# Kernel optimization log

Measured on AMD Instinct MI355X. Metric: run time of the kernel, lower is better.

The kernel has to match this reference:

```python
import jax, jax.numpy as jnp
import numpy as np

D = 128      # dim_hidden
L = 8        # topological levels (level 0 = primary inputs)
M = 32768    # nodes per level
N = L * M
G = 5        # gate types: maj/not/and/or/xor -> 5 param sets
F = 2        # fan-in per gate node


def setup_inputs() -> dict:
    key = jax.random.key(0)
    ks = jax.random.split(key, 18)
    p = lambda k, sh: jax.random.normal(k, sh, jnp.float32) * 0.05
    return {
        's': jax.random.normal(ks[0], (N, D), jnp.float32),
        't': jax.random.normal(ks[1], (N, D), jnp.float32),
        'gate': jax.random.randint(ks[2], (N,), 0, G, jnp.int32),
        'fanin': jax.random.randint(ks[3], (L - 1, M, F), 0, M, jnp.int32),
        'hs_W': p(ks[4], (2 * D, D)), 'hs_b': p(ks[5], (D,)),
        'aggr_W1': p(ks[6], (G, 2 * D, D)), 'aggr_b1': p(ks[7], (G, D)),
        'aggr_W2': p(ks[8], (G, D, D)), 'aggr_b2': p(ks[9], (G, D)),
        'aggr_W3': p(ks[10], (G, D, D)), 'aggr_b3': p(ks[11], (G, D)),
        'gru_Wi': p(ks[12], (G, D, 3 * D)), 'gru_Wh': p(ks[13], (G, D, 3 * D)),
        'gru_bi': p(ks[14], (G, 3 * D)), 'gru_bh': p(ks[15], (G, 3 * D)),
    }


def _forward(s, t, gate, fanin, hs_W, hs_b, aggr_W1, aggr_b1, aggr_W2, aggr_b2,
             aggr_W3, aggr_b3, gru_Wi, gru_Wh, gru_bi, gru_bh):
    hs = jnp.concatenate([s, t], -1) @ hs_W + hs_b          # [N,D]
    hf = jnp.zeros((N, D), hs.dtype)                        # functional state, zero-init
    for lvl in range(1, L):                                 # level-synchronous sweep
        lo = lvl * M
        g_l = gate[lo:lo + M]                               # [M] gate type of dst nodes
        oh = jax.nn.one_hot(g_l, G, dtype=hs.dtype)         # [M,G] gate selector
        src = (lvl - 1) * M + fanin[lvl - 1]                # [M,F] global fan-in indices
        src_state = jnp.concatenate([hs[src], hf[src]], -1)  # [M,F,2D] node_state gather
        # per-gate-type edge MLP (TFMlpAggr): 3-layer MLP on source states, sum over fan-in
        h1 = jax.nn.relu(jnp.einsum('mfc,gcd->gmfd', src_state, aggr_W1) + aggr_b1[:, None, None, :])
        h2 = jax.nn.relu(jnp.einsum('gmfd,gde->gmfe', h1, aggr_W2) + aggr_b2[:, None, None, :])
        m = jnp.einsum('gmfe,gek->gmfk', h2, aggr_W3) + aggr_b3[:, None, None, :]
        msg = jnp.einsum('gmd,mg->md', m.sum(axis=2), oh)   # [M,D] select own gate's aggr
        # per-gate-type GRU update of hf (torch GRU math, seq_len=1)
        h = hf[lo:lo + M]                                   # [M,D]
        gi = jnp.einsum('md,gdk->gmk', msg, gru_Wi) + gru_bi[:, None, :]  # [G,M,3D]
        gh = jnp.einsum('md,gdk->gmk', h, gru_Wh) + gru_bh[:, None, :]
        r = jax.nn.sigmoid(gi[..., :D] + gh[..., :D])
        z = jax.nn.sigmoid(gi[..., D:2 * D] + gh[..., D:2 * D])
        n = jnp.tanh(gi[..., 2 * D:] + r * gh[..., 2 * D:])
        h_new = jnp.einsum('gmd,mg->md', (1.0 - z) * n + z * h[None], oh)
        hf = hf.at[lo:lo + M].set(h_new)                    # scatter-write back
    return hs, hf


def reference(s, t, gate, fanin, hs_W, hs_b, aggr_W1, aggr_b1, aggr_W2, aggr_b2,
              aggr_W3, aggr_b3, gru_Wi, gru_Wh, gru_bi, gru_bh):
    return _forward(s, t, gate, fanin, hs_W, hs_b, aggr_W1, aggr_b1, aggr_W2,
                    aggr_b2, aggr_W3, aggr_b3, gru_Wi, gru_Wh, gru_bi, gru_bh)
```

## Files before the change

### kernel.cpp

```cpp
#include <hip/hip_runtime.h>
#include <hip/hip_bf16.h>

#define DD 128
#define LL 8
#define MM 32768
#define NN (LL*MM)
#define GG 5
#define FF 2
#define SORT_STRIDE 33408

typedef __attribute__((ext_vector_type(8))) short short8;
typedef __attribute__((ext_vector_type(4))) short short4v;
typedef __attribute__((ext_vector_type(4))) float f32x4;

#define MFMA16(a,b,c) __builtin_amdgcn_mfma_f32_16x16x32_bf16((a),(b),(c),0,0,0)
#define VMEM_FENCE() asm volatile("s_waitcnt vmcnt(0)" ::: "memory")

__device__ __forceinline__ short f2bf(float x){
  __hip_bfloat16 h = __float2bfloat16(x);
  return *reinterpret_cast<short*>(&h);
}

__device__ __forceinline__ short8 pack8(f32x4 a, f32x4 b){
  short8 r;
  r[0]=f2bf(a[0]); r[1]=f2bf(a[1]); r[2]=f2bf(a[2]); r[3]=f2bf(a[3]);
  r[4]=f2bf(b[0]); r[5]=f2bf(b[1]); r[6]=f2bf(b[2]); r[7]=f2bf(b[3]);
  return r;
}

__global__ void prep_kernel(const float* __restrict__ hs_W, const float* __restrict__ W1,
                            const float* __restrict__ W2, const float* __restrict__ W3,
                            const float* __restrict__ Wi,
                            short* __restrict__ hsWt, short* __restrict__ W1t,
                            short* __restrict__ W2t, short* __restrict__ W3t,
                            short* __restrict__ Wit, int* __restrict__ cntcur)
{
  if (blockIdx.x == 0 && threadIdx.x < 70) cntcur[threadIdx.x] = 0;
  int u = blockIdx.x*256 + threadIdx.x;
  const float* src; short* dst; int ldw;
  if (u < 4096){
    int i=u, ct=i>>9, kc=(i>>6)&7, ln=i&63;
    src = hs_W + (size_t)(kc*32 + 8*(ln>>4))*128 + ct*16 + (ln&15);
    dst = hsWt + (size_t)i*8; ldw=128;
  } else if (u < 24576){
    int v=u-4096, g=v>>12, i=v&4095, ct=i>>9, kc=(i>>6)&7, ln=i&63;
    src = W1 + (size_t)g*32768 + (size_t)(kc*32 + 8*(ln>>4))*128 + ct*16 + (ln&15);
    dst = W1t + (size_t)g*32768 + i*8; ldw=128;
  } else if (u < 34816){
    int v=u-24576, g=v>>11, i=v&2047, ct=i>>8, kc=(i>>6)&3, ln=i&63;
    src = W2 + (size_t)g*16384 + (size_t)(kc*32 + 8*(ln>>4))*128 + ct*16 + (ln&15);
    dst = W2t + (size_t)g*16384 + i*8; ldw=128;
  } else if (u < 45056){
    int v=u-34816, g=v>>11, i=v&2047, ct=i>>8, kc=(i>>6)&3, ln=i&63;
    src = W3 + (size_t)g*16384 + (size_t)(kc*32 + 8*(ln>>4))*128 + ct*16 + (ln&15);
    dst = W3t + (size_t)g*16384 + i*8; ldw=128;
  } else {
    int v=u-45056, g=v/6144, i=v%6144, ct=i>>8, kc=(i>>6)&3, ln=i&63;
    src = Wi + (size_t)g*49152 + (size_t)(kc*32 + 8*(ln>>4))*384 + ct*16 + (ln&15);
    dst = Wit + (size_t)g*49152 + i*8; ldw=384;
  }
  short8 o;
#pragma unroll
  for (int j=0;j<8;++j) o[j] = f2bf(src[(size_t)j*ldw]);
  *(short8*)dst = o;
}

__global__ void count_kernel(const int* __restrict__ gate, int* __restrict__ cnt){
  __shared__ int lc[GG];
  const int li = blockIdx.x >> 7;
  const int m  = ((blockIdx.x & 127) << 8) + threadIdx.x;
  if (threadIdx.x < GG) lc[threadIdx.x] = 0;
  __syncthreads();
  int g = gate[(li+1)*MM + m];
  atomicAdd(&lc[g], 1);
  __syncthreads();
  if (threadIdx.x < GG && lc[threadIdx.x] > 0)
    atomicAdd(&cnt[li*GG + threadIdx.x], lc[threadIdx.x]);
}

__global__ void offs_kernel(const int* __restrict__ cnt, int* __restrict__ off,
                            int* __restrict__ pend, int* __restrict__ sorted){
  __shared__ int se[35], sp[35];
  const int tid = threadIdx.x;
  if (tid < LL-1){
    int l = tid, o = 0;
    for (int g = 0; g < GG; ++g){
      off[l*GG+g] = o;
      int c = cnt[l*GG+g];
      pend[l*GG+g] = o + c;
      se[l*GG+g] = o + c;
      o += ((c + 31) >> 5) << 5;
      sp[l*GG+g] = o;
    }
  }
  __syncthreads();
  for (int b = 0; b < 35; ++b){
    int l = b / GG;
    for (int i = se[b] + tid; i < sp[b]; i += 256)
      sorted[l*SORT_STRIDE + i] = -1;
  }
}

__global__ void scatter_kernel(const int* __restrict__ gate, const int* __restrict__ off,
                               int* __restrict__ cur, int* __restrict__ sorted){
  __shared__ int lc[GG];
  __shared__ int base[GG];
  const int li = blockIdx.x >> 7;
  const int m  = ((blockIdx.x & 127) << 8) + threadIdx.x;
  if (threadIdx.x < GG) lc[threadIdx.x] = 0;
  __syncthreads();
  int g = gate[(li+1)*MM + m];
  int p = atomicAdd(&lc[g], 1);
  __syncthreads();
  if (threadIdx.x < GG)
    base[threadIdx.x] = atomicAdd(&cur[li*GG + threadIdx.x], lc[threadIdx.x]);
  __syncthreads();
  sorted[li*SORT_STRIDE + off[li*GG+g] + base[g] + p] = m;
}

__global__ __launch_bounds__(256,5) void hs_kernel(
    const float* __restrict__ s, const float* __restrict__ t,
    const short* __restrict__ Wt, const float* __restrict__ b,
    float* __restrict__ hs, short* __restrict__ xsh,
    float* __restrict__ hf)
{
  __shared__ __align__(16) short Xs[16384];
  const int tid=threadIdx.x, lane=tid&63, w=tid>>6;
  const int l15=lane&15, lq=lane>>4;
  const int row0 = blockIdx.x*64;

  {
    const int r = tid>>2, p = tid&3;
    const float* srow = s + (size_t)(row0+r)*DD;
    const float* trow = t + (size_t)(row0+r)*DD;
    const int rf = r>>4, rl = r&15;
#pragma unroll
    for (int h=0; h<2; ++h){
      f32x4 va[8];
#pragma unroll
      for (int i=0;i<4;++i){
        int u = p + 4*(4*h + i);
        const float* pp = (u<16) ? (srow + 8*u) : (trow + 8*(u-16));
        va[2*i]   = __builtin_nontemporal_load((const f32x4*)pp);
        va[2*i+1] = __builtin_nontemporal_load((const f32x4*)(pp+4));
      }
      VMEM_FENCE();
#pragma unroll
      for (int i=0;i<4;++i){
        int u = p + 4*(4*h + i);
        short8 v = pack8(va[2*i], va[2*i+1]);
        *(short8*)(Xs + ((rf*8+(u>>2))*64 + (u&3)*16 + rl)*8) = v;
      }
    }
  }

  if (row0 < MM){
    f32x4 zf4 = {0.f,0.f,0.f,0.f};
    short8 zs8 = {0,0,0,0,0,0,0,0};
    const size_t basei = (size_t)row0*DD;
    for (int i=tid; i<2048; i+=256)
      __builtin_nontemporal_store(zf4, (f32x4*)(hf + basei + i*4));
    for (int i=tid; i<1024; i+=256)
      *(short8*)(xsh + ((size_t)row0 + (i>>4))*256 + 128 + (i&15)*8) = zs8;
  }
  __syncthreads();

  f32x4 zf = {0.f,0.f,0.f,0.f};
  f32x4 acc[4][2];
#pragma unroll
  for (int rr=0;rr<4;++rr){ acc[rr][0]=zf; acc[rr][1]=zf; }
  const short* Aw = Wt + (16*w)*512 + lane*8;
#pragma unroll
  for (int h=0; h<2; ++h){
    short8 af[8];
#pragma unroll
    for (int i=0;i<8;++i) af[i] = *(const short8*)(Aw + (8*h + i)*512);
    VMEM_FENCE();
#pragma unroll
    for (int kc=0;kc<8;++kc){
      short8 bx[4];
#pragma unroll
      for (int rr=0;rr<4;++rr)
        bx[rr] = *(const short8*)(Xs + ((rr*8 + kc)*64 + lane)*8);
#pragma unroll
      for (int rr=0;rr<4;++rr)
        acc[rr][h] = MFMA16(af[kc], bx[rr], acc[rr][h]);
    }
  }

  f32x4 bv0 = *(const f32x4*)(b + 32*w + 4*lq);
  f32x4 bv1 = *(const f32x4*)(b + 32*w + 16 + 4*lq);
#pragma unroll
  for (int rr=0;rr<4;++rr){
    int row = row0 + rr*16 + l15;
#pragma unroll
    for (int q=0;q<2;++q){
      f32x4 bv = q ? bv1 : bv0;
      int col = 32*w + 16*q + 4*lq;
      f32x4 o; short4v pk;
#pragma unroll
      for (int j=0;j<4;++j){ o[j] = acc[rr][q][j] + bv[j]; pk[j] = f2bf(o[j]); }
      __builtin_nontemporal_store(o, (f32x4*)(hs + (size_t)row*DD + col));
      *(short4v*)(xsh + (size_t)row*256 + col) = pk;
    }
  }
}

__global__ __launch_bounds__(256,5) void level_kernel(
    int lvl, float* __restrict__ hfg, short* __restrict__ xsh,
    const int* __restrict__ fanin,
    const short* __restrict__ W1t, const short* __restrict__ W2t,
    const short* __restrict__ W3t, const short* __restrict__ Wit,
    const float* __restrict__ b1, const float* __restrict__ b2,
    const float* __restrict__ b3, const float* __restrict__ bi,
    const float* __restrict__ bh,
    const int* __restrict__ off, const int* __restrict__ pend,
    const int* __restrict__ sorted)
{
  __shared__ __align__(16) short Xs[16384];
  const int tid=threadIdx.x, lane=tid&63, w=tid>>6;
  const int l15=lane&15, lq=lane>>4;
  const int li = lvl-1;

  const int bid = blockIdx.x;
  const int xcd = bid & 7, idx = bid >> 3;
  const int nbid = ((xcd < 4) ? xcd*131 : 524 + (xcd-4)*130) + idx;
  const int pos0 = nbid*32;

  int g = -1;
#pragma unroll
  for (int q=0;q<GG;++q)
    if (pos0 >= off[li*GG+q] && pos0 < pend[li*GG+q]) g = q;
  if (g < 0) return;

  const int m0 = sorted[li*SORT_STRIDE + pos0 + l15];
  const int m1 = sorted[li*SORT_STRIDE + pos0 + 16 + l15];
  f32x4 zf = {0.f,0.f,0.f,0.f};

  {
    const int r = tid>>2, p = tid&3;
    const int mg = sorted[li*SORT_STRIDE + pos0 + (r>>1)];
    const int src = (mg>=0) ? li*MM + fanin[((size_t)li*MM+mg)*FF + (r&1)] : 0;
    const short* xrow = xsh + (size_t)src*256;
    const int rf = r>>4, rl = r&15;
    const bool lvl1 = (lvl == 1);
    short8 va[8];
    short8 zs8 = {0,0,0,0,0,0,0,0};
#pragma unroll
    for (int i=0;i<8;++i){
      int u = p + 4*i;
      va[i] = (lvl1 && u >= 16) ? zs8 : *(const short8*)(xrow + 8*u);
    }
    VMEM_FENCE();
#pragma unroll
    for (int i=0;i<8;++i){
      int u = p + 4*i;
      *(short8*)(Xs + ((rf*8+(u>>2))*64 + (u&3)*16 + rl)*8) = va[i];
    }
  }
  __syncthreads();

  f32x4 acc[4][2];
#pragma unroll
  for (int rr=0;rr<4;++rr){ acc[rr][0]=zf; acc[rr][1]=zf; }
  {
    const short* A1w = W1t + (size_t)g*32768 + (16*w)*512 + lane*8;
#pragma unroll
    for (int h=0; h<2; ++h){
      short8 af[8];
#pragma unroll
      for (int i=0;i<8;++i) af[i] = *(const short8*)(A1w + (8*h + i)*512);
      VMEM_FENCE();
#pragma unroll
      for (int kc=0;kc<8;++kc){
        short8 bx[4];
#pragma unroll
        for (int rr=0;rr<4;++rr)
          bx[rr] = *(const short8*)(Xs + ((rr*8 + kc)*64 + lane)*8);
#pragma unroll
        for (int rr=0;rr<4;++rr)
          acc[rr][h] = MFMA16(af[kc], bx[rr], acc[rr][h]);
      }
    }
  }
  __syncthreads();
  {
    f32x4 bv0 = *(const f32x4*)(b1 + g*DD + 32*w + 4*lq);
    f32x4 bv1 = *(const f32x4*)(b1 + g*DD + 32*w + 16 + 4*lq);
#pragma unroll
    for (int rr=0;rr<4;++rr){
#pragma unroll
      for (int q=0;q<2;++q){
        f32x4 bv = q ? bv1 : bv0;
        short4v pk;
#pragma unroll
        for (int j=0;j<4;++j) pk[j] = f2bf(fmaxf(acc[rr][q][j] + bv[j], 0.f));
        *(short4v*)(Xs + ((rr*4 + w)*64 + (2*q + (lq>>1))*16 + l15)*8 + 4*(lq&1)) = pk;
      }
    }
  }
  __syncthreads();

  f32x4 acc2[4][2];
#pragma unroll
  for (int rr=0;rr<4;++rr){ acc2[rr][0]=zf; acc2[rr][1]=zf; }
  {
    const short* A2w = W2t + (size_t)g*16384 + (8*w)*512 + lane*8;
    short8 af[8];
#pragma unroll
    for (int i=0;i<8;++i) af[i] = *(const short8*)(A2w + i*512);
    VMEM_FENCE();
#pragma unroll
    for (int kc=0;kc<4;++kc){
      short8 bx[4];
#pragma unroll
      for (int rr=0;rr<4;++rr)
        bx[rr] = *(const short8*)(Xs + ((rr*4 + kc)*64 + lane)*8);
#pragma unroll
      for (int rr=0;rr<4;++rr){
        acc2[rr][0] = MFMA16(af[kc],   bx[rr], acc2[rr][0]);
        acc2[rr][1] = MFMA16(af[4+kc], bx[rr], acc2[rr][1]);
      }
    }
  }
  {
    f32x4 bv0 = *(const f32x4*)(b2 + g*DD + 32*w + 4*lq);
    f32x4 bv1 = *(const f32x4*)(b2 + g*DD + 32*w + 16 + 4*lq);
#pragma unroll
    for (int rr=0;rr<4;++rr){
#pragma unroll
      for (int q=0;q<2;++q){
        f32x4 bv = q ? bv1 : bv0;
        short4v pk;
#pragma unroll
        for (int j=0;j<4;++j) pk[j] = f2bf(fmaxf(acc2[rr][q][j] + bv[j], 0.f));
        *(short4v*)(Xs + 8192 + ((rr*4 + w)*64 + (2*q + (lq>>1))*16 + l15)*8 + 4*(lq&1)) = pk;
      }
    }
  }
  __syncthreads();

  f32x4 acc3[4][2];
#pragma unroll
  for (int rr=0;rr<4;++rr){ acc3[rr][0]=zf; acc3[rr][1]=zf; }
  {
    const short* A3w = W3t + (size_t)g*16384 + (8*w)*512 + lane*8;
    short8 af[8];
#pragma unroll
    for (int i=0;i<8;++i) af[i] = *(const short8*)(A3w + i*512);
    VMEM_FENCE();
#pragma unroll
    for (int kc=0;kc<4;++kc){
      short8 bx[4];
#pragma unroll
      for (int rr=0;rr<4;++rr)
        bx[rr] = *(const short8*)(Xs + 8192 + ((rr*4 + kc)*64 + lane)*8);
#pragma unroll
      for (int rr=0;rr<4;++rr){
        acc3[rr][0] = MFMA16(af[kc],   bx[rr], acc3[rr][0]);
        acc3[rr][1] = MFMA16(af[4+kc], bx[rr], acc3[rr][1]);
      }
    }
  }
  {
    f32x4 bv0 = *(const f32x4*)(b3 + g*DD + 32*w + 4*lq);
    f32x4 bv1 = *(const f32x4*)(b3 + g*DD + 32*w + 16 + 4*lq);
#pragma unroll
    for (int rr=0;rr<4;++rr){
#pragma unroll
      for (int q=0;q<2;++q){
        f32x4 bv = q ? bv1 : bv0;
        f32x4 mv;
#pragma unroll
        for (int j=0;j<4;++j){
          float v = acc3[rr][q][j];
          mv[j] = v + __shfl_xor(v, 1) + 2.f*bv[j];
        }
        if ((l15 & 1) == 0){
          int n = rr*8 + (l15>>1);
          short4v pk;
#pragma unroll
          for (int j=0;j<4;++j) pk[j] = f2bf(mv[j]);
          *(short4v*)(Xs + (((n>>4)*4 + w)*64 + (2*q + (lq>>1))*16 + (n&15))*8 + 4*(lq&1)) = pk;
        }
      }
    }
  }
  __syncthreads();

  const short* AW = Wit + (size_t)g*49152 + lane*8;
  const int lo = lvl*MM;
#pragma unroll
  for (int q=0;q<2;++q){
    short8 af[12];
#pragma unroll
    for (int kc=0;kc<4;++kc){
      int cti = ((2*w + q)*4 + kc)*512;
      af[kc]   = *(const short8*)(AW + cti);
      af[4+kc] = *(const short8*)(AW + 16384 + cti);
      af[8+kc] = *(const short8*)(AW + 32768 + cti);
    }
    VMEM_FENCE();
    f32x4 gr[2], gz[2], gn[2];
    gr[0]=zf; gr[1]=zf; gz[0]=zf; gz[1]=zf; gn[0]=zf; gn[1]=zf;
#pragma unroll
    for (int kc=0;kc<4;++kc){
#pragma unroll
      for (int rfm=0;rfm<2;++rfm){
        short8 bm = *(const short8*)(Xs + ((rfm*4 + kc)*64 + lane)*8);
        gr[rfm] = MFMA16(af[kc],   bm, gr[rfm]);
        gz[rfm] = MFMA16(af[4+kc], bm, gz[rfm]);
        gn[rfm] = MFMA16(af[8+kc], bm, gn[rfm]);
      }
    }
    int col = 32*w + 16*q + 4*lq;
    f32x4 biR = *(const f32x4*)(bi + g*384 + col);
    f32x4 biZ = *(const f32x4*)(bi + g*384 + 128 + col);
    f32x4 biN = *(const f32x4*)(bi + g*384 + 256 + col);
    f32x4 bhR = *(const f32x4*)(bh + g*384 + col);
    f32x4 bhZ = *(const f32x4*)(bh + g*384 + 128 + col);
    f32x4 bhN = *(const f32x4*)(bh + g*384 + 256 + col);
#pragma unroll
    for (int rfm=0;rfm<2;++rfm){
      int m = rfm ? m1 : m0;
      if (m < 0) continue;
      f32x4 o; short4v pk;
#pragma unroll
      for (int j=0;j<4;++j){
        float xr = gr[rfm][j] + biR[j] + bhR[j];
        float xz = gz[rfm][j] + biZ[j] + bhZ[j];
        float r_ = 1.f/(1.f + __expf(-xr));
        float z_ = 1.f/(1.f + __expf(-xz));
        float xn = gn[rfm][j] + biN[j] + r_*bhN[j];
        float n_ = 2.f/(1.f + __expf(-2.f*xn)) - 1.f;
        o[j] = (1.f - z_)*n_;
        pk[j] = f2bf(o[j]);
      }
      __builtin_nontemporal_store(o, (f32x4*)(hfg + (size_t)(lo + m)*DD + col));
      *(short4v*)(xsh + (size_t)(lo + m)*256 + 128 + col) = pk;
    }
  }
}

extern "C" void kernel_launch(void* const* d_in, const int* in_sizes, int n_in,
                              void* d_out, int out_size, void* d_ws, size_t ws_size,
                              hipStream_t stream)
{
  const float* s    = (const float*)d_in[0];
  const float* t    = (const float*)d_in[1];
  const int*   gate = (const int*)d_in[2];
  const int*   fanin= (const int*)d_in[3];
  const float* hs_W = (const float*)d_in[4];
  const float* hs_b = (const float*)d_in[5];
  const float* W1   = (const float*)d_in[6];
  const float* b1   = (const float*)d_in[7];
  const float* W2   = (const float*)d_in[8];
  const float* b2   = (const float*)d_in[9];
  const float* W3   = (const float*)d_in[10];
  const float* b3   = (const float*)d_in[11];
  const float* Wi   = (const float*)d_in[12];
  const float* bi   = (const float*)d_in[14];
  const float* bh   = (const float*)d_in[15];

  float* hs = (float*)d_out;
  float* hf = hs + (size_t)NN*DD;

  int* cnt    = (int*)d_ws;
  int* cur    = cnt + 35;
  int* off    = cnt + 70;
  int* pendv  = cnt + 105;
  int* sorted = cnt + 256;

  short* wbase = (short*)((char*)d_ws + (1<<20));
  short* hsWt = wbase;
  short* W1t  = wbase + 32768;
  short* W2t  = wbase + 196608;
  short* W3t  = wbase + 278528;
  short* Wit  = wbase + 360448;

  short* xsh = (short*)((char*)d_ws + (size_t)(8<<20));

  prep_kernel<<<296, 256, 0, stream>>>(hs_W, W1, W2, W3, Wi,
                                       hsWt, W1t, W2t, W3t, Wit, cnt);
  count_kernel<<<896, 256, 0, stream>>>(gate, cnt);
  offs_kernel<<<1, 256, 0, stream>>>(cnt, off, pendv, sorted);
  scatter_kernel<<<896, 256, 0, stream>>>(gate, off, cur, sorted);
  hs_kernel<<<NN/64, 256, 0, stream>>>(s, t, hsWt, hs_b, hs, xsh, hf);
  for (int lvl = 1; lvl < LL; ++lvl){
    level_kernel<<<SORT_STRIDE/32, 256, 0, stream>>>(lvl, hf, xsh,
        fanin, W1t, W2t, W3t, Wit,
        b1, b2, b3, bi, bh, off, pendv, sorted);
  }
}
```

Baseline: 378.8 us.

## Process two row tiles per block, prefetching second gather during first compute

Each level-kernel block now handles two consecutive 32-node tiles instead of one, with a halved grid and an adjusted XCD-aware block remapping. The fan-in gather for the second tile is issued into registers before the first tile's MLP+GRU chain runs, so its memory latency overlaps with the first tile's compute. Launch bounds drop from 5 to 4 blocks per CU to make room for the extra prefetch registers, which lowers occupancy and leaves fewer blocks to hide latency.

```diff
diff --git a/kernel.cpp b/kernel.cpp
--- a/kernel.cpp
+++ b/kernel.cpp
@@ -206,7 +206,7 @@
   }
 }
 
-__global__ __launch_bounds__(256,5) void level_kernel(
+__global__ __launch_bounds__(256,4) void level_kernel(
     int lvl, float* __restrict__ hfg, short* __restrict__ xsh,
     const int* __restrict__ fanin,
     const short* __restrict__ W1t, const short* __restrict__ W2t,
@@ -224,221 +224,247 @@
 
   const int bid = blockIdx.x;
   const int xcd = bid & 7, idx = bid >> 3;
-  const int nbid = ((xcd < 4) ? xcd*131 : 524 + (xcd-4)*130) + idx;
-  const int pos0 = nbid*32;
-
-  int g = -1;
-#pragma unroll
-  for (int q=0;q<GG;++q)
-    if (pos0 >= off[li*GG+q] && pos0 < pend[li*GG+q]) g = q;
-  if (g < 0) return;
-
-  const int m0 = sorted[li*SORT_STRIDE + pos0 + l15];
-  const int m1 = sorted[li*SORT_STRIDE + pos0 + 16 + l15];
+  const int nbid = ((xcd < 2) ? xcd*66 : 132 + (xcd-2)*65) + idx;
+  const int pos0 = nbid*64;
+
+  auto lookup_g = [&](int pos) -> int {
+    int g = -1;
+#pragma unroll
+    for (int q=0;q<GG;++q)
+      if (pos >= off[li*GG+q] && pos < pend[li*GG+q]) g = q;
+    return g;
+  };
+  const int g0 = lookup_g(pos0);
+  const int g1 = lookup_g(pos0 + 32);
+
+  const int r = tid>>2, p = tid&3;
+  const int rf = r>>4, rl = r&15;
+  const bool lvl1 = (lvl == 1);
   f32x4 zf = {0.f,0.f,0.f,0.f};
-
-  {
-    const int r = tid>>2, p = tid&3;
-    const int mg = sorted[li*SORT_STRIDE + pos0 + (r>>1)];
+  short8 zs8 = {0,0,0,0,0,0,0,0};
+
+  auto gather_issue = [&](int pos, short8* va){
+    const int mg = sorted[li*SORT_STRIDE + pos + (r>>1)];
     const int src = (mg>=0) ? li*MM + fanin[((size_t)li*MM+mg)*FF + (r&1)] : 0;
     const short* xrow = xsh + (size_t)src*256;
-    const int rf = r>>4, rl = r&15;
-    const bool lvl1 = (lvl == 1);
-    short8 va[8];
-    short8 zs8 = {0,0,0,0,0,0,0,0};
 #pragma unroll
     for (int i=0;i<8;++i){
       int u = p + 4*i;
       va[i] = (lvl1 && u >= 16) ? zs8 : *(const short8*)(xrow + 8*u);
     }
-    VMEM_FENCE();
+  };
+  auto write_xs = [&](const short8* va){
 #pragma unroll
     for (int i=0;i<8;++i){
       int u = p + 4*i;
       *(short8*)(Xs + ((rf*8+(u>>2))*64 + (u&3)*16 + rl)*8) = va[i];
     }
-  }
-  __syncthreads();
-
-  f32x4 acc[4][2];
-#pragma unroll
-  for (int rr=0;rr<4;++rr){ acc[rr][0]=zf; acc[rr][1]=zf; }
-  {
-    const short* A1w = W1t + (size_t)g*32768 + (16*w)*512 + lane*8;
-#pragma unroll
-    for (int h=0; h<2; ++h){
+  };
+
+  auto compute_item = [&](int g, int pos){
+    const int m0 = sorted[li*SORT_STRIDE + pos + l15];
+    const int m1 = sorted[li*SORT_STRIDE + pos + 16 + l15];
+
+    f32x4 acc[4][2];
+#pragma unroll
+    for (int rr=0;rr<4;++rr){ acc[rr][0]=zf; acc[rr][1]=zf; }
+    {
+      const short* A1w = W1t + (size_t)g*32768 + (16*w)*512 + lane*8;
+#pragma unroll
+      for (int h=0; h<2; ++h){
+        short8 af[8];
+#pragma unroll
+        for (int i=0;i<8;++i) af[i] = *(const short8*)(A1w + (8*h + i)*512);
+        VMEM_FENCE();
+#pragma unroll
+        for (int kc=0;kc<8;++kc){
+          short8 bx[4];
+#pragma unroll
+          for (int rr=0;rr<4;++rr)
+            bx[rr] = *(const short8*)(Xs + ((rr*8 + kc)*64 + lane)*8);
+#pragma unroll
+          for (int rr=0;rr<4;++rr)
+            acc[rr][h] = MFMA16(af[kc], bx[rr], acc[rr][h]);
+        }
+      }
+    }
+    __syncthreads();
+    {
+      f32x4 bv0 = *(const f32x4*)(b1 + g*DD + 32*w + 4*lq);
+      f32x4 bv1 = *(const f32x4*)(b1 + g*DD + 32*w + 16 + 4*lq);
+#pragma unroll
+      for (int rr=0;rr<4;++rr){
+#pragma unroll
+        for (int q=0;q<2;++q){
+          f32x4 bv = q ? bv1 : bv0;
+          short4v pk;
+#pragma unroll
+          for (int j=0;j<4;++j) pk[j] = f2bf(fmaxf(acc[rr][q][j] + bv[j], 0.f));
+          *(short4v*)(Xs + ((rr*4 + w)*64 + (2*q + (lq>>1))*16 + l15)*8 + 4*(lq&1)) = pk;
+        }
+      }
+    }
+    __syncthreads();
+
+    f32x4 acc2[4][2];
+#pragma unroll
+    for (int rr=0;rr<4;++rr){ acc2[rr][0]=zf; acc2[rr][1]=zf; }
+    {
+      const short* A2w = W2t + (size_t)g*16384 + (8*w)*512 + lane*8;
       short8 af[8];
 #pragma unroll
-      for (int i=0;i<8;++i) af[i] = *(const short8*)(A1w + (8*h + i)*512);
+      for (int i=0;i<8;++i) af[i] = *(const short8*)(A2w + i*512);
       VMEM_FENCE();
 #pragma unroll
-      for (int kc=0;kc<8;++kc){
+      for (int kc=0;kc<4;++kc){
         short8 bx[4];
 #pragma unroll
         for (int rr=0;rr<4;++rr)
-          bx[rr] = *(const short8*)(Xs + ((rr*8 + kc)*64 + lane)*8);
+          bx[rr] = *(const short8*)(Xs + ((rr*4 + kc)*64 + lane)*8);
+#pragma unroll
+        for (int rr=0;rr<4;++rr){
+          acc2[rr][0] = MFMA16(af[kc],   bx[rr], acc2[rr][0]);
+          acc2[rr][1] = MFMA16(af[4+kc], bx[rr], acc2[rr][1]);
+        }
+      }
+    }
+    {
+      f32x4 bv0 = *(const f32x4*)(b2 + g*DD + 32*w + 4*lq);
+      f32x4 bv1 = *(const f32x4*)(b2 + g*DD + 32*w + 16 + 4*lq);
+#pragma unroll
+      for (int rr=0;rr<4;++rr){
+#pragma unroll
+        for (int q=0;q<2;++q){
+          f32x4 bv = q ? bv1 : bv0;
+          short4v pk;
+#pragma unroll
+          for (int j=0;j<4;++j) pk[j] = f2bf(fmaxf(acc2[rr][q][j] + bv[j], 0.f));
+          *(short4v*)(Xs + 8192 + ((rr*4 + w)*64 + (2*q + (lq>>1))*16 + l15)*8 + 4*(lq&1)) = pk;
+        }
+      }
+    }
+    __syncthreads();
+
+    f32x4 acc3[4][2];
+#pragma unroll
+    for (int rr=0;rr<4;++rr){ acc3[rr][0]=zf; acc3[rr][1]=zf; }
+    {
+      const short* A3w = W3t + (size_t)g*16384 + (8*w)*512 + lane*8;
+      short8 af[8];
+#pragma unroll
+      for (int i=0;i<8;++i) af[i] = *(const short8*)(A3w + i*512);
+      VMEM_FENCE();
+#pragma unroll
+      for (int kc=0;kc<4;++kc){
+        short8 bx[4];
 #pragma unroll
         for (int rr=0;rr<4;++rr)
-          acc[rr][h] = MFMA16(af[kc], bx[rr], acc[rr][h]);
-      }
-    }
-  }
-  __syncthreads();
-  {
-    f32x4 bv0 = *(const f32x4*)(b1 + g*DD + 32*w + 4*lq);
-    f32x4 bv1 = *(const f32x4*)(b1 + g*DD + 32*w + 16 + 4*lq);
-#pragma unroll
-    for (int rr=0;rr<4;++rr){
-#pragma unroll
-      for (int q=0;q<2;++q){
-        f32x4 bv = q ? bv1 : bv0;
-        short4v pk;
-#pragma unroll
-        for (int j=0;j<4;++j) pk[j] = f2bf(fmaxf(acc[rr][q][j] + bv[j], 0.f));
-        *(short4v*)(Xs + ((rr*4 + w)*64 + (2*q + (lq>>1))*16 + l15)*8 + 4*(lq&1)) = pk;
-      }
-    }
-  }
-  __syncthreads();
-
-  f32x4 acc2[4][2];
-#pragma unroll
-  for (int rr=0;rr<4;++rr){ acc2[rr][0]=zf; acc2[rr][1]=zf; }
-  {
-    const short* A2w = W2t + (size_t)g*16384 + (8*w)*512 + lane*8;
-    short8 af[8];
-#pragma unroll
-    for (int i=0;i<8;++i) af[i] = *(const short8*)(A2w + i*512);
+          bx[rr] = *(const short8*)(Xs + 8192 + ((rr*4 + kc)*64 + lane)*8);
+#pragma unroll
+        for (int rr=0;rr<4;++rr){
+          acc3[rr][0] = MFMA16(af[kc],   bx[rr], acc3[rr][0]);
+          acc3[rr][1] = MFMA16(af[4+kc], bx[rr], acc3[rr][1]);
+        }
+      }
+    }
+    {
+      f32x4 bv0 = *(const f32x4*)(b3 + g*DD + 32*w + 4*lq);
+      f32x4 bv1 = *(const f32x4*)(b3 + g*DD + 32*w + 16 + 4*lq);
+#pragma unroll
+      for (int rr=0;rr<4;++rr){
+#pragma unroll
+        for (int q=0;q<2;++q){
+          f32x4 bv = q ? bv1 : bv0;
+          f32x4 mv;
+#pragma unroll
+          for (int j=0;j<4;++j){
+            float v = acc3[rr][q][j];
+            mv[j] = v + __shfl_xor(v, 1) + 2.f*bv[j];
+          }
+          if ((l15 & 1) == 0){
+            int n = rr*8 + (l15>>1);
+            short4v pk;
+#pragma unroll
+            for (int j=0;j<4;++j) pk[j] = f2bf(mv[j]);
+            *(short4v*)(Xs + (((n>>4)*4 + w)*64 + (2*q + (lq>>1))*16 + (n&15))*8 + 4*(lq&1)) = pk;
+          }
+        }
+      }
+    }
+    __syncthreads();
+
+    const short* AW = Wit + (size_t)g*49152 + lane*8;
+    const int lo = lvl*MM;
+#pragma unroll
+    for (int q=0;q<2;++q){
+      short8 af[12];
+#pragma unroll
+      for (int kc=0;kc<4;++kc){
+        int cti = ((2*w + q)*4 + kc)*512;
+        af[kc]   = *(const short8*)(AW + cti);
+        af[4+kc] = *(const short8*)(AW + 16384 + cti);
+        af[8+kc] = *(const short8*)(AW + 32768 + cti);
+      }
+      VMEM_FENCE();
+      f32x4 gr[2], gz[2], gn[2];
+      gr[0]=zf; gr[1]=zf; gz[0]=zf; gz[1]=zf; gn[0]=zf; gn[1]=zf;
+#pragma unroll
+      for (int kc=0;kc<4;++kc){
+#pragma unroll
+        for (int rfm=0;rfm<2;++rfm){
+          short8 bm = *(const short8*)(Xs + ((rfm*4 + kc)*64 + lane)*8);
+          gr[rfm] = MFMA16(af[kc],   bm, gr[rfm]);
+          gz[rfm] = MFMA16(af[4+kc], bm, gz[rfm]);
+          gn[rfm] = MFMA16(af[8+kc], bm, gn[rfm]);
+        }
+      }
+      int col = 32*w + 16*q + 4*lq;
+      f32x4 biR = *(const f32x4*)(bi + g*384 + col);
+      f32x4 biZ = *(const f32x4*)(bi + g*384 + 128 + col);
+      f32x4 biN = *(const f32x4*)(bi + g*384 + 256 + col);
+      f32x4 bhR = *(const f32x4*)(bh + g*384 + col);
+      f32x4 bhZ = *(const f32x4*)(bh + g*384 + 128 + col);
+      f32x4 bhN = *(const f32x4*)(bh + g*384 + 256 + col);
+#pragma unroll
+      for (int rfm=0;rfm<2;++rfm){
+        int m = rfm ? m1 : m0;
+        if (m < 0) continue;
+        f32x4 o; short4v pk;
+#pragma unroll
+        for (int j=0;j<4;++j){
+          float xr = gr[rfm][j] + biR[j] + bhR[j];
+          float xz = gz[rfm][j] + biZ[j] + bhZ[j];
+          float r_ = 1.f/(1.f + __expf(-xr));
+          float z_ = 1.f/(1.f + __expf(-xz));
+          float xn = gn[rfm][j] + biN[j] + r_*bhN[j];
+          float n_ = 2.f/(1.f + __expf(-2.f*xn)) - 1.f;
+          o[j] = (1.f - z_)*n_;
+          pk[j] = f2bf(o[j]);
+        }
+        __builtin_nontemporal_store(o, (f32x4*)(hfg + (size_t)(lo + m)*DD + col));
+        *(short4v*)(xsh + (size_t)(lo + m)*256 + 128 + col) = pk;
+      }
+    }
+  };
+
+  short8 va[8];
+  if (g0 >= 0){
+    gather_issue(pos0, va);
     VMEM_FENCE();
-#pragma unroll
-    for (int kc=0;kc<4;++kc){
-      short8 bx[4];
-#pragma unroll
-      for (int rr=0;rr<4;++rr)
-        bx[rr] = *(const short8*)(Xs + ((rr*4 + kc)*64 + lane)*8);
-#pragma unroll
-      for (int rr=0;rr<4;++rr){
-        acc2[rr][0] = MFMA16(af[kc],   bx[rr], acc2[rr][0]);
-        acc2[rr][1] = MFMA16(af[4+kc], bx[rr], acc2[rr][1]);
-      }
-    }
-  }
-  {
-    f32x4 bv0 = *(const f32x4*)(b2 + g*DD + 32*w + 4*lq);
-    f32x4 bv1 = *(const f32x4*)(b2 + g*DD + 32*w + 16 + 4*lq);
-#pragma unroll
-    for (int rr=0;rr<4;++rr){
-#pragma unroll
-      for (int q=0;q<2;++q){
-        f32x4 bv = q ? bv1 : bv0;
-        short4v pk;
-#pragma unroll
-        for (int j=0;j<4;++j) pk[j] = f2bf(fmaxf(acc2[rr][q][j] + bv[j], 0.f));
-        *(short4v*)(Xs + 8192 + ((rr*4 + w)*64 + (2*q + (lq>>1))*16 + l15)*8 + 4*(lq&1)) = pk;
-      }
-    }
-  }
-  __syncthreads();
-
-  f32x4 acc3[4][2];
-#pragma unroll
-  for (int rr=0;rr<4;++rr){ acc3[rr][0]=zf; acc3[rr][1]=zf; }
-  {
-    const short* A3w = W3t + (size_t)g*16384 + (8*w)*512 + lane*8;
-    short8 af[8];
-#pragma unroll
-    for (int i=0;i<8;++i) af[i] = *(const short8*)(A3w + i*512);
+    write_xs(va);
+  }
+  __syncthreads();
+  if (g1 >= 0){
+    gather_issue(pos0 + 32, va);
+    __builtin_amdgcn_sched_barrier(0);
+  }
+  if (g0 >= 0) compute_item(g0, pos0);
+  __syncthreads();
+  if (g1 >= 0){
     VMEM_FENCE();
-#pragma unroll
-    for (int kc=0;kc<4;++kc){
-      short8 bx[4];
-#pragma unroll
-      for (int rr=0;rr<4;++rr)
-        bx[rr] = *(const short8*)(Xs + 8192 + ((rr*4 + kc)*64 + lane)*8);
-#pragma unroll
-      for (int rr=0;rr<4;++rr){
-        acc3[rr][0] = MFMA16(af[kc],   bx[rr], acc3[rr][0]);
-        acc3[rr][1] = MFMA16(af[4+kc], bx[rr], acc3[rr][1]);
-      }
-    }
-  }
-  {
-    f32x4 bv0 = *(const f32x4*)(b3 + g*DD + 32*w + 4*lq);
-    f32x4 bv1 = *(const f32x4*)(b3 + g*DD + 32*w + 16 + 4*lq);
-#pragma unroll
-    for (int rr=0;rr<4;++rr){
-#pragma unroll
-      for (int q=0;q<2;++q){
-        f32x4 bv = q ? bv1 : bv0;
-        f32x4 mv;
-#pragma unroll
-        for (int j=0;j<4;++j){
-          float v = acc3[rr][q][j];
-          mv[j] = v + __shfl_xor(v, 1) + 2.f*bv[j];
-        }
-        if ((l15 & 1) == 0){
-          int n = rr*8 + (l15>>1);
-          short4v pk;
-#pragma unroll
-          for (int j=0;j<4;++j) pk[j] = f2bf(mv[j]);
-          *(short4v*)(Xs + (((n>>4)*4 + w)*64 + (2*q + (lq>>1))*16 + (n&15))*8 + 4*(lq&1)) = pk;
-        }
-      }
-    }
-  }
-  __syncthreads();
-
-  const short* AW = Wit + (size_t)g*49152 + lane*8;
-  const int lo = lvl*MM;
-#pragma unroll
-  for (int q=0;q<2;++q){
-    short8 af[12];
-#pragma unroll
-    for (int kc=0;kc<4;++kc){
-      int cti = ((2*w + q)*4 + kc)*512;
-      af[kc]   = *(const short8*)(AW + cti);
-      af[4+kc] = *(const short8*)(AW + 16384 + cti);
-      af[8+kc] = *(const short8*)(AW + 32768 + cti);
-    }
-    VMEM_FENCE();
-    f32x4 gr[2], gz[2], gn[2];
-    gr[0]=zf; gr[1]=zf; gz[0]=zf; gz[1]=zf; gn[0]=zf; gn[1]=zf;
-#pragma unroll
-    for (int kc=0;kc<4;++kc){
-#pragma unroll
-      for (int rfm=0;rfm<2;++rfm){
-        short8 bm = *(const short8*)(Xs + ((rfm*4 + kc)*64 + lane)*8);
-        gr[rfm] = MFMA16(af[kc],   bm, gr[rfm]);
-        gz[rfm] = MFMA16(af[4+kc], bm, gz[rfm]);
-        gn[rfm] = MFMA16(af[8+kc], bm, gn[rfm]);
-      }
-    }
-    int col = 32*w + 16*q + 4*lq;
-    f32x4 biR = *(const f32x4*)(bi + g*384 + col);
-    f32x4 biZ = *(const f32x4*)(bi + g*384 + 128 + col);
-    f32x4 biN = *(const f32x4*)(bi + g*384 + 256 + col);
-    f32x4 bhR = *(const f32x4*)(bh + g*384 + col);
-    f32x4 bhZ = *(const f32x4*)(bh + g*384 + 128 + col);
-    f32x4 bhN = *(const f32x4*)(bh + g*384 + 256 + col);
-#pragma unroll
-    for (int rfm=0;rfm<2;++rfm){
-      int m = rfm ? m1 : m0;
-      if (m < 0) continue;
-      f32x4 o; short4v pk;
-#pragma unroll
-      for (int j=0;j<4;++j){
-        float xr = gr[rfm][j] + biR[j] + bhR[j];
-        float xz = gz[rfm][j] + biZ[j] + bhZ[j];
-        float r_ = 1.f/(1.f + __expf(-xr));
-        float z_ = 1.f/(1.f + __expf(-xz));
-        float xn = gn[rfm][j] + biN[j] + r_*bhN[j];
-        float n_ = 2.f/(1.f + __expf(-2.f*xn)) - 1.f;
-        o[j] = (1.f - z_)*n_;
-        pk[j] = f2bf(o[j]);
-      }
-      __builtin_nontemporal_store(o, (f32x4*)(hfg + (size_t)(lo + m)*DD + col));
-      *(short4v*)(xsh + (size_t)(lo + m)*256 + 128 + col) = pk;
-    }
+    write_xs(va);
+    __syncthreads();
+    compute_item(g1, pos0 + 32);
   }
 }
 
@@ -487,7 +513,7 @@
   scatter_kernel<<<896, 256, 0, stream>>>(gate, off, cur, sorted);
   hs_kernel<<<NN/64, 256, 0, stream>>>(s, t, hsWt, hs_b, hs, xsh, hf);
   for (int lvl = 1; lvl < LL; ++lvl){
-    level_kernel<<<SORT_STRIDE/32, 256, 0, stream>>>(lvl, hf, xsh,
+    level_kernel<<<SORT_STRIDE/64, 256, 0, stream>>>(lvl, hf, xsh,
         fanin, W1t, W2t, W3t, Wit,
         b1, b2, b3, bi, bh, off, pendv, sorted);
   }
```

After: 409.5 us. 8.1% more time.
